# Kernel optimization log

Measured on AMD Instinct MI355X. Metric: run time of the kernel, lower is better.

The kernel has to match this reference:

```python
import jax, jax.numpy as jnp
import numpy as np

N = 1_000_000          # points
C_IN = 10              # decorated point features
C_OUT = 64             # pillar feature channels
S = 30_000             # number of pillars (segments)
EPS = 1e-3             # BatchNorm1d eps


def setup_inputs() -> dict:
    key = jax.random.key(0)
    ks = jax.random.split(key, 8)
    inputs = jax.random.normal(ks[0], (N, C_IN), dtype=jnp.float32)
    # every pillar gets ~N/S points; sorted, all segments non-empty
    unq_inv = jnp.sort(jnp.arange(N, dtype=jnp.int32) % S)
    W_lin = jax.random.normal(ks[1], (C_OUT, C_IN), dtype=jnp.float32) * 0.3
    gamma = 1.0 + 0.1 * jax.random.normal(ks[2], (C_OUT,), dtype=jnp.float32)
    beta = 0.1 * jax.random.normal(ks[3], (C_OUT,), dtype=jnp.float32)
    dw1 = jax.random.normal(ks[4], (C_OUT,), dtype=jnp.float32) * 0.5      # depthwise 1x1 conv (groups=C)
    pw1 = jax.random.normal(ks[5], (C_OUT, C_OUT), dtype=jnp.float32) * 0.1  # pointwise 1x1 conv
    dw2 = jax.random.normal(ks[6], (C_OUT,), dtype=jnp.float32) * 0.5
    pw2 = jax.random.normal(ks[7], (C_OUT, C_OUT), dtype=jnp.float32) * 0.1
    return {"inputs": inputs, "unq_inv": unq_inv, "W_lin": W_lin,
            "gamma": gamma, "beta": beta, "dw1": dw1, "pw1": pw1,
            "dw2": dw2, "pw2": pw2}


def reference(inputs, unq_inv, W_lin, gamma, beta, dw1, pw1, dw2, pw2):
    # Linear (no bias) -> BN (training-mode batch stats) -> ReLU
    x = inputs @ W_lin.T                                   # [N, C]
    mu = jnp.mean(x, axis=0)
    var = jnp.mean(jnp.square(x - mu), axis=0)             # biased var, as torch BN
    x = (x - mu) * jax.lax.rsqrt(var + EPS) * gamma + beta
    x = jax.nn.relu(x)

    # MAFF attention: local branch (depthwise scale -> swish -> 1x1 conv)
    s = x * dw1                                            # groups=C 1x1 conv == per-channel scale
    xl = (s * jax.nn.sigmoid(s)) @ pw1.T                   # [N, C]
    # global branch: avg-pool over points -> depthwise scale -> relu -> 1x1 conv
    g = jnp.mean(x, axis=0)                                # [C]
    xg = pw2 @ jax.nn.relu(dw2 * g)                        # [C]
    wei = jax.nn.sigmoid(xl + xg)                          # broadcast [N,C] + [C]
    xi = x * (1.0 + wei)

    # segment reductions keyed by pillar id (scatter_max + scatter_sum)
    x_max = jax.ops.segment_max(xi, unq_inv, num_segments=S,
                                indices_are_sorted=True)
    x_sum = jax.ops.segment_sum(xi, unq_inv, num_segments=S,
                                indices_are_sorted=True)
    return x_max + x_sum                                   # [S, C]
```

## Files before the change

kernel.cpp:

```cpp
#include <hip/hip_runtime.h>
#include <math.h>

#define N_PTS   1000000
#define CI      10
#define C       64
#define NSEG    30000
#define BN_EPS  1e-3f
#define FROFF   31104


using f32x4 = __attribute__((ext_vector_type(4))) float;
using s16x8 = __attribute__((ext_vector_type(8))) short;

__device__ inline short f2bf(float x) {
    unsigned u = __float_as_uint(x);
    unsigned r = (u + 0x7fffu + ((u >> 16) & 1u)) >> 16;
    return (short)r;
}
__device__ inline unsigned pack_trunc(float lo, float hi) {
    return (__float_as_uint(hi) & 0xffff0000u) | (__float_as_uint(lo) >> 16);
}
__device__ inline float frcp(float x) { return __builtin_amdgcn_rcpf(x); }
__device__ inline void lds_fence() {
    asm volatile("s_waitcnt lgkmcnt(0)" ::: "memory");
}

__global__ void __launch_bounds__(256) k_moments(const float* __restrict__ inp,
                                                 const int* __restrict__ idx,
                                                 float* __restrict__ ws,
                                                 int* __restrict__ starts) {
    const int tid = threadIdx.x;
    float v[65];
#pragma unroll
    for (int k = 0; k < 65; ++k) v[k] = 0.f;

    for (int p = blockIdx.x * blockDim.x + tid; p < N_PTS; p += gridDim.x * blockDim.x) {
        const float2* r2 = (const float2*)(inp + (size_t)p * CI);
        float2 a0 = r2[0], a1 = r2[1], a2 = r2[2], a3 = r2[3], a4 = r2[4];
        float r[CI] = {a0.x, a0.y, a1.x, a1.y, a2.x, a2.y, a3.x, a3.y, a4.x, a4.y};
#pragma unroll
        for (int i = 0; i < CI; ++i) v[i] += r[i];
        int kk = 10;
#pragma unroll
        for (int i = 0; i < CI; ++i)
#pragma unroll
            for (int j = i; j < CI; ++j) { v[kk] = fmaf(r[i], r[j], v[kk]); ++kk; }

        int iv = idx[p];
        if (p == 0) starts[0] = 0;
        else if (idx[p - 1] != iv) starts[iv] = p;
    }

#pragma unroll
    for (int k = 0; k < 65; ++k) {
#pragma unroll
        for (int off = 32; off >= 1; off >>= 1)
            v[k] += __shfl_xor(v[k], off, 64);
    }
    __shared__ float red[4 * 65];
    const int wv = tid >> 6, ln = tid & 63;
    if (ln == 0) {
#pragma unroll
        for (int k = 0; k < 65; ++k) red[wv * 65 + k] = v[k];
    }
    __syncthreads();
    if (tid < 65)
        atomicAdd(&ws[tid], red[tid] + red[65 + tid] + red[130 + tid] + red[195 + tid]);
}

__global__ void __launch_bounds__(256) k_gstats(const float* __restrict__ inp,
                                                const float* __restrict__ W,
                                                const float* __restrict__ gamma,
                                                const float* __restrict__ beta,
                                                float* __restrict__ ws) {
    const int tid  = threadIdx.x;
    const int wv   = tid >> 6;
    const int lane = tid & 63;
    const int m = lane & 15;
    const int q = lane >> 4;

    __shared__ float wp[C * CI];
    __shared__ float bsh[C];

    if (tid < C) {
        const int c = tid;
        float w[CI];
#pragma unroll
        for (int i = 0; i < CI; ++i) w[i] = W[c * CI + i];
        const float inv_n = 1.f / (float)N_PTS;

        float mu = 0.f;
#pragma unroll
        for (int i = 0; i < CI; ++i) mu = fmaf(w[i], ws[i], mu);
        mu *= inv_n;

        float ex2 = 0.f;
        int kk = 10;
#pragma unroll
        for (int i = 0; i < CI; ++i)
#pragma unroll
            for (int j = i; j < CI; ++j) {
                float mm = ws[kk];
                float t = w[i] * w[j] * mm;
                ex2 += (i == j) ? t : 2.f * t;
                ++kk;
            }
        ex2 *= inv_n;

        float var = ex2 - mu * mu;
        float rstd = rsqrtf(var + BN_EPS);
        float a = rstd * gamma[c];
        float b = beta[c] - mu * a;
        bsh[c] = b;
#pragma unroll
        for (int i = 0; i < CI; ++i) wp[c * CI + i] = a * w[i];
    }
    __syncthreads();

    s16x8 wfr[4];
#pragma unroll
    for (int nt = 0; nt < 4; ++nt) {
        s16x8 t;
#pragma unroll
        for (int j = 0; j < 8; ++j) {
            int k = 8 * q + j;
            t[j] = (k < CI) ? f2bf(wp[(nt * 16 + m) * CI + k]) : (short)0;
        }
        wfr[nt] = t;
    }
    float bb[4];
#pragma unroll
    for (int nt = 0; nt < 4; ++nt) bb[nt] = bsh[nt * 16 + m];

    const int wid = blockIdx.x * 4 + wv;
    const int nw  = gridDim.x * 4;
    const int NB  = N_PTS / 16;

    float2 P0, P1, P2, P3;
    auto loadrows = [&](int pb) {
        const float* row = inp + (size_t)(pb + m) * CI;
        if (q == 0) {
            P0 = *(const float2*)(row);     P1 = *(const float2*)(row + 2);
            P2 = *(const float2*)(row + 4); P3 = *(const float2*)(row + 6);
        } else if (q == 1) {
            P0 = *(const float2*)(row + 8);
        }
    };
    P0 = P1 = P2 = P3 = make_float2(0.f, 0.f);

    float sm[4] = {0.f, 0.f, 0.f, 0.f};
    const f32x4 zero = {0.f, 0.f, 0.f, 0.f};

    if (wid < NB) loadrows(wid * 16);
    for (int b = wid; b < NB; b += nw) {
        float2 L0 = P0, L1 = P1, L2 = P2, L3 = P3;
        if (b + nw < NB) loadrows((b + nw) * 16);

        union { s16x8 v; unsigned u[4]; } t;
        t.v = s16x8{0, 0, 0, 0, 0, 0, 0, 0};
        if (q < 2) t.u[0] = pack_trunc(L0.x, L0.y);
        if (q == 0) {
            t.u[1] = pack_trunc(L1.x, L1.y);
            t.u[2] = pack_trunc(L2.x, L2.y);
            t.u[3] = pack_trunc(L3.x, L3.y);
        }

        f32x4 xt[4];
#pragma unroll
        for (int nt = 0; nt < 4; ++nt) {
            xt[nt] = __builtin_amdgcn_mfma_f32_16x16x32_bf16(t.v, wfr[nt], zero, 0, 0, 0);
#pragma unroll
            for (int r = 0; r < 4; ++r)
                sm[nt] += fmaxf(xt[nt][r] + bb[nt], 0.f);
        }
    }

#pragma unroll
    for (int nt = 0; nt < 4; ++nt) {
        sm[nt] += __shfl_xor(sm[nt], 16, 64);
        sm[nt] += __shfl_xor(sm[nt], 32, 64);
    }
    float S = sm[0];
    if (q == 1) S = sm[1];
    if (q == 2) S = sm[2];
    if (q == 3) S = sm[3];

    __shared__ float red[4 * 64];
    red[wv * 64 + lane] = S;
    __syncthreads();
    if (tid < 64)
        atomicAdd(&ws[256 + tid], red[tid] + red[64 + tid] + red[128 + tid] + red[192 + tid]);
}

__global__ void k_prep(const float* __restrict__ W,
                       const float* __restrict__ gamma,
                       const float* __restrict__ beta,
                       const float* __restrict__ dw1,
                       const float* __restrict__ pw1,
                       const float* __restrict__ dw2,
                       const float* __restrict__ pw2,
                       float* __restrict__ ws) {
    const int lane = threadIdx.x;
    const int m = lane & 15, q = lane >> 4;
    const float inv_n = 1.f / (float)N_PTS;

    __shared__ float WP[C * CI];
    __shared__ float BSH[C], T[C], XG[C];

    {
        float w[CI];
#pragma unroll
        for (int i = 0; i < CI; ++i) w[i] = W[lane * CI + i];
        float mu = 0.f;
#pragma unroll
        for (int i = 0; i < CI; ++i) mu = fmaf(w[i], ws[i], mu);
        mu *= inv_n;
        float ex2 = 0.f;
        int kk = 10;
#pragma unroll
        for (int i = 0; i < CI; ++i)
#pragma unroll
            for (int j = i; j < CI; ++j) {
                float mm = ws[kk];
                float t = w[i] * w[j] * mm;
                ex2 += (i == j) ? t : 2.f * t;
                ++kk;
            }
        ex2 *= inv_n;
        float var = ex2 - mu * mu;
        float rstd = rsqrtf(var + BN_EPS);
        float a = rstd * gamma[lane];
        BSH[lane] = beta[lane] - mu * a;
#pragma unroll
        for (int i = 0; i < CI; ++i) WP[lane * CI + i] = a * w[i];
        T[lane] = fmaxf(dw2[lane] * (ws[256 + lane] * inv_n), 0.f);
    }
    __syncthreads();

    {
        float acc = 0.f;
#pragma unroll
        for (int k = 0; k < C; ++k) acc = fmaf(pw2[lane * C + k], T[k], acc);
        XG[lane] = acc;
    }
    __syncthreads();

    float4* FR = (float4*)(ws + FROFF);
    union { float4 f; s16x8 v; } u;

#pragma unroll
    for (int nt = 0; nt < 4; ++nt) {
        s16x8 tt;
#pragma unroll
        for (int j = 0; j < 8; ++j) {
            int k = 8 * q + j;
            tt[j] = (k < CI) ? f2bf(WP[(nt * 16 + m) * CI + k]) : (short)0;
        }
        u.v = tt; FR[nt * 64 + lane] = u.f;
    }
#pragma unroll
    for (int nt = 0; nt < 4; ++nt)
#pragma unroll
        for (int kc = 0; kc < 2; ++kc) {
            const float* src = pw1 + (nt * 16 + m) * C + kc * 32 + q * 8;
            float4 p0 = *(const float4*)src, p1 = *(const float4*)(src + 4);
            s16x8 tt;
            tt[0] = f2bf(p0.x); tt[1] = f2bf(p0.y); tt[2] = f2bf(p0.z); tt[3] = f2bf(p0.w);
            tt[4] = f2bf(p1.x); tt[5] = f2bf(p1.y); tt[6] = f2bf(p1.z); tt[7] = f2bf(p1.w);
            u.v = tt; FR[(4 + nt * 2 + kc) * 64 + lane] = u.f;
        }
    float4 f;
    f.x = BSH[m]; f.y = BSH[16 + m]; f.z = BSH[32 + m]; f.w = BSH[48 + m];
    FR[12 * 64 + lane] = f;
    f.x = dw1[m]; f.y = dw1[16 + m]; f.z = dw1[32 + m]; f.w = dw1[48 + m];
    FR[13 * 64 + lane] = f;
    f.x = XG[m]; f.y = XG[16 + m]; f.z = XG[32 + m]; f.w = XG[48 + m];
    FR[14 * 64 + lane] = f;
}

#define LD 68
#define SEGW 2
struct Rows { float2 r0, r1, r2, r3; };
__global__ void __launch_bounds__(128) k_main(const float* __restrict__ inp,
                                              const float* __restrict__ ws,
                                              const int* __restrict__ starts,
                                              float* __restrict__ out) {
    const int tid  = threadIdx.x;
    const int wv   = tid >> 6;
    const int lane = tid & 63;
    const int m = lane & 15;
    const int q = lane >> 4;
    const f32x4 zero = {0.f, 0.f, 0.f, 0.f};

    const float4* FR = (const float4*)(ws + FROFF);
    union { float4 f; s16x8 v; } u;
    s16x8 wfr[4];
#pragma unroll
    for (int nt = 0; nt < 4; ++nt) { u.f = FR[nt * 64 + lane]; wfr[nt] = u.v; }
    s16x8 bfr[4][2];
#pragma unroll
    for (int nt = 0; nt < 4; ++nt)
#pragma unroll
        for (int kc = 0; kc < 2; ++kc) { u.f = FR[(4 + nt * 2 + kc) * 64 + lane]; bfr[nt][kc] = u.v; }
    const float4 bb4  = FR[12 * 64 + lane];
    const float4 d14  = FR[13 * 64 + lane];
    const float4 xg4  = FR[14 * 64 + lane];
    const float bb[4]  = {bb4.x, bb4.y, bb4.z, bb4.w};
    const float d1v[4] = {d14.x, d14.y, d14.z, d14.w};
    const float xgv[4] = {xg4.x, xg4.y, xg4.z, xg4.w};

    __shared__ float sb[2][16 * LD];
    float* my = sb[wv];

    const int w  = blockIdx.x * 2 + wv;
    const int s0 = w * SEGW;

    int st1 = starts[s0 + 1];
    int st2 = (s0 + 2 < NSEG) ? starts[s0 + 2] : N_PTS;
    const int start   = starts[s0];
    const int end_all = st2;

    int cur = s0;
    int end_cur = st1;

    float sm[4]  = {0.f, 0.f, 0.f, 0.f};
    float mxv[4] = {-INFINITY, -INFINITY, -INFINITY, -INFINITY};

    auto flushseg = [&](int s) {
#pragma unroll
        for (int nt = 0; nt < 4; ++nt) {
            sm[nt] += __shfl_xor(sm[nt], 16, 64);
            sm[nt] += __shfl_xor(sm[nt], 32, 64);
            mxv[nt] = fmaxf(mxv[nt], __shfl_xor(mxv[nt], 16, 64));
            mxv[nt] = fmaxf(mxv[nt], __shfl_xor(mxv[nt], 32, 64));
        }
        float S = sm[0], M = mxv[0];
        if (q == 1) { S = sm[1]; M = mxv[1]; }
        if (q == 2) { S = sm[2]; M = mxv[2]; }
        if (q == 3) { S = sm[3]; M = mxv[3]; }
        out[(size_t)s * C + lane] = S + M;
#pragma unroll
        for (int nt = 0; nt < 4; ++nt) { sm[nt] = 0.f; mxv[nt] = -INFINITY; }
    };

    auto loadrows = [&](int pb) -> Rows {
        Rows R;
        R.r0 = R.r1 = R.r2 = R.r3 = make_float2(0.f, 0.f);
        const float* row = inp + (size_t)min(pb + m, N_PTS - 1) * CI;
        if (q == 0) {
            R.r0 = *(const float2*)(row);     R.r1 = *(const float2*)(row + 2);
            R.r2 = *(const float2*)(row + 4); R.r3 = *(const float2*)(row + 6);
        } else if (q == 1) {
            R.r0 = *(const float2*)(row + 8);
        }
        return R;
    };

    Rows A = loadrows(start);
    Rows B = (start + 16 < end_all) ? loadrows(start + 16) : A;

    for (int base = start; base < end_all; base += 16) {
        Rows L = A;
        A = B;
        if (base + 32 < end_all) B = loadrows(base + 32);

        const int nb = min(16, end_all - base);

        union { s16x8 v; unsigned u[4]; } t;
        t.v = s16x8{0, 0, 0, 0, 0, 0, 0, 0};
        if (q < 2) t.u[0] = pack_trunc(L.r0.x, L.r0.y);
        if (q == 0) {
            t.u[1] = pack_trunc(L.r1.x, L.r1.y);
            t.u[2] = pack_trunc(L.r2.x, L.r2.y);
            t.u[3] = pack_trunc(L.r3.x, L.r3.y);
        }

        f32x4 xt[4];
#pragma unroll
        for (int nt = 0; nt < 4; ++nt)
            xt[nt] = __builtin_amdgcn_mfma_f32_16x16x32_bf16(t.v, wfr[nt], zero, 0, 0, 0);

        float xn[4][4];
#pragma unroll
        for (int nt = 0; nt < 4; ++nt)
#pragma unroll
            for (int r = 0; r < 4; ++r) {
                float x = fmaxf(xt[nt][r] + bb[nt], 0.f);
                xn[nt][r] = x;
                float sg = x * d1v[nt];
                float sw = sg * frcp(1.f + __expf(-sg));
                my[(4 * q + r) * LD + nt * 16 + m] = sw;
            }
        lds_fence();

        s16x8 av[2];
#pragma unroll
        for (int kc = 0; kc < 2; ++kc) {
            const float* src = &my[m * LD + kc * 32 + q * 8];
            float4 p0 = *(const float4*)src;
            float4 p1 = *(const float4*)(src + 4);
            union { s16x8 v; unsigned u[4]; } tt;
            tt.u[0] = pack_trunc(p0.x, p0.y);
            tt.u[1] = pack_trunc(p0.z, p0.w);
            tt.u[2] = pack_trunc(p1.x, p1.y);
            tt.u[3] = pack_trunc(p1.z, p1.w);
            av[kc] = tt.v;
        }

        f32x4 xi[4];
#pragma unroll
        for (int nt = 0; nt < 4; ++nt) {
            xi[nt] = __builtin_amdgcn_mfma_f32_16x16x32_bf16(av[0], bfr[nt][0], zero, 0, 0, 0);
            xi[nt] = __builtin_amdgcn_mfma_f32_16x16x32_bf16(av[1], bfr[nt][1], xi[nt], 0, 0, 0);
        }
        lds_fence();

#pragma unroll
        for (int nt = 0; nt < 4; ++nt)
#pragma unroll
            for (int r = 0; r < 4; ++r) {
                float v   = xi[nt][r] + xgv[nt];
                float wei = frcp(1.f + __expf(-v));
                float x   = xn[nt][r];
                xi[nt][r] = fmaf(x, wei, x);
            }

        const int fin = base + nb;
        if (fin <= end_cur) {
            if (nb == 16) {
#pragma unroll
                for (int nt = 0; nt < 4; ++nt)
#pragma unroll
                    for (int r = 0; r < 4; ++r) {
                        sm[nt] += xi[nt][r];
                        mxv[nt] = fmaxf(mxv[nt], xi[nt][r]);
                    }
            } else {
#pragma unroll
                for (int nt = 0; nt < 4; ++nt)
#pragma unroll
                    for (int r = 0; r < 4; ++r) {
                        bool act = (4 * q + r) < nb;
                        sm[nt] += act ? xi[nt][r] : 0.f;
                        mxv[nt] = fmaxf(mxv[nt], act ? xi[nt][r] : -INFINITY);
                    }
            }
            if (fin == end_cur) { flushseg(cur); ++cur; end_cur = st2; }
        } else {
            const int B = end_cur - base;
#pragma unroll
            for (int nt = 0; nt < 4; ++nt)
#pragma unroll
                for (int r = 0; r < 4; ++r) {
                    bool act = (4 * q + r) < B;
                    sm[nt] += act ? xi[nt][r] : 0.f;
                    mxv[nt] = fmaxf(mxv[nt], act ? xi[nt][r] : -INFINITY);
                }
            flushseg(cur); ++cur;
#pragma unroll
            for (int nt = 0; nt < 4; ++nt)
#pragma unroll
                for (int r = 0; r < 4; ++r) {
                    int pt = 4 * q + r;
                    bool act = (pt >= B) && (pt < nb);
                    sm[nt] += act ? xi[nt][r] : 0.f;
                    mxv[nt] = fmaxf(mxv[nt], act ? xi[nt][r] : -INFINITY);
                }
            end_cur = st2;
        }
    }
}

extern "C" void kernel_launch(void* const* d_in, const int* in_sizes, int n_in,
                              void* d_out, int out_size, void* d_ws, size_t ws_size,
                              hipStream_t stream) {
    const float* inp   = (const float*)d_in[0];
    const int*   unq   = (const int*)d_in[1];
    const float* W     = (const float*)d_in[2];
    const float* gamma = (const float*)d_in[3];
    const float* beta  = (const float*)d_in[4];
    const float* dw1   = (const float*)d_in[5];
    const float* pw1   = (const float*)d_in[6];
    const float* dw2   = (const float*)d_in[7];
    const float* pw2   = (const float*)d_in[8];
    float* out = (float*)d_out;
    float* ws  = (float*)d_ws;
    int* starts = (int*)ws + 1024;

    hipMemsetAsync(ws, 0, 384 * sizeof(float), stream);

    k_moments <<<1024, 256, 0, stream>>>(inp, unq, ws, starts);
    k_gstats  <<<1024, 256, 0, stream>>>(inp, W, gamma, beta, ws);
    k_prep    <<<1,    64,  0, stream>>>(W, gamma, beta, dw1, pw1, dw2, pw2, ws);
    k_main    <<<7500, 128, 0, stream>>>(inp, ws, starts, out);
}
```

Measured before the change: 268.2 us.

## Replace atomic reductions with per-block partials and two-stage reductions

The moments and global-stats kernels now write per-block partial sums to workspace instead of using atomicAdd. A separate reduction kernel sums the moment partials, and the prep kernel, widened to 1024 threads, sums the gstats partials. This removes the memset and the atomic contention. Separately, the grids grow to 2048 blocks, k_moments processes two points per thread with float4 loads, k_gstats uses double-buffered prefetch, and one LDS fence in k_main is dropped. In exchange it adds an extra kernel launch, and dropping the fence risks an LDS race.

```diff
diff --git a/kernel.cpp b/kernel.cpp
--- a/kernel.cpp
+++ b/kernel.cpp
@@ -6,7 +6,13 @@
 #define C       64
 #define NSEG    30000
 #define BN_EPS  1e-3f
-#define FROFF   31104
+
+#define NBLK_M  2048
+#define NBLK_G  2048
+#define P1STR   72
+#define P1OFF   32768
+#define P2OFF   (P1OFF + NBLK_M * P1STR)
+#define FROFF   (P2OFF + NBLK_G * 64)
 
 
 using f32x4 = __attribute__((ext_vector_type(4))) float;
@@ -23,6 +29,11 @@
 __device__ inline float frcp(float x) { return __builtin_amdgcn_rcpf(x); }
 __device__ inline void lds_fence() {
     asm volatile("s_waitcnt lgkmcnt(0)" ::: "memory");
+}
+
+struct Rows { float2 r0, r1, r2, r3; };
+__device__ inline Rows zrows() {
+    Rows R; R.r0 = R.r1 = R.r2 = R.r3 = make_float2(0.f, 0.f); return R;
 }
 
 __global__ void __launch_bounds__(256) k_moments(const float* __restrict__ inp,
@@ -34,21 +45,29 @@
 #pragma unroll
     for (int k = 0; k < 65; ++k) v[k] = 0.f;
 
-    for (int p = blockIdx.x * blockDim.x + tid; p < N_PTS; p += gridDim.x * blockDim.x) {
-        const float2* r2 = (const float2*)(inp + (size_t)p * CI);
-        float2 a0 = r2[0], a1 = r2[1], a2 = r2[2], a3 = r2[3], a4 = r2[4];
-        float r[CI] = {a0.x, a0.y, a1.x, a1.y, a2.x, a2.y, a3.x, a3.y, a4.x, a4.y};
-#pragma unroll
-        for (int i = 0; i < CI; ++i) v[i] += r[i];
+    const int NPP = N_PTS / 2;
+    for (int pp = blockIdx.x * blockDim.x + tid; pp < NPP; pp += gridDim.x * blockDim.x) {
+        const float4* base = (const float4*)(inp + (size_t)pp * 20);
+        float4 a = base[0], b4 = base[1], c = base[2], d = base[3], e = base[4];
+        float r0[CI] = {a.x, a.y, a.z, a.w, b4.x, b4.y, b4.z, b4.w, c.x, c.y};
+        float r1[CI] = {c.z, c.w, d.x, d.y, d.z, d.w, e.x, e.y, e.z, e.w};
+#pragma unroll
+        for (int i = 0; i < CI; ++i) v[i] += r0[i] + r1[i];
         int kk = 10;
 #pragma unroll
         for (int i = 0; i < CI; ++i)
 #pragma unroll
-            for (int j = i; j < CI; ++j) { v[kk] = fmaf(r[i], r[j], v[kk]); ++kk; }
-
-        int iv = idx[p];
-        if (p == 0) starts[0] = 0;
-        else if (idx[p - 1] != iv) starts[iv] = p;
+            for (int j = i; j < CI; ++j) {
+                v[kk] = fmaf(r0[i], r0[j], v[kk]);
+                v[kk] = fmaf(r1[i], r1[j], v[kk]);
+                ++kk;
+            }
+
+        const int p0 = 2 * pp;
+        int2 iv = *(const int2*)(idx + p0);
+        if (p0 == 0) starts[0] = 0;
+        else { int prev = idx[p0 - 1]; if (prev != iv.x) starts[iv.x] = p0; }
+        if (iv.x != iv.y) starts[iv.y] = p0 + 1;
     }
 
 #pragma unroll
@@ -65,7 +84,24 @@
     }
     __syncthreads();
     if (tid < 65)
-        atomicAdd(&ws[tid], red[tid] + red[65 + tid] + red[130 + tid] + red[195 + tid]);
+        ws[P1OFF + blockIdx.x * P1STR + tid] =
+            red[tid] + red[65 + tid] + red[130 + tid] + red[195 + tid];
+}
+
+__global__ void __launch_bounds__(256) k_red(float* __restrict__ ws) {
+    const int k = blockIdx.x;
+    float s = 0.f;
+    for (int i = threadIdx.x; i < NBLK_M; i += 256)
+        s += ws[P1OFF + i * P1STR + k];
+    __shared__ float r[256];
+    r[threadIdx.x] = s;
+    __syncthreads();
+#pragma unroll
+    for (int off = 128; off > 0; off >>= 1) {
+        if (threadIdx.x < off) r[threadIdx.x] += r[threadIdx.x + off];
+        __syncthreads();
+    }
+    if (threadIdx.x == 0) ws[k] = r[0];
 }
 
 __global__ void __launch_bounds__(256) k_gstats(const float* __restrict__ inp,
@@ -78,6 +114,7 @@
     const int lane = tid & 63;
     const int m = lane & 15;
     const int q = lane >> 4;
+    const float inv_n = 1.f / (float)N_PTS;
 
     __shared__ float wp[C * CI];
     __shared__ float bsh[C];
@@ -87,13 +124,10 @@
         float w[CI];
 #pragma unroll
         for (int i = 0; i < CI; ++i) w[i] = W[c * CI + i];
-        const float inv_n = 1.f / (float)N_PTS;
-
         float mu = 0.f;
 #pragma unroll
         for (int i = 0; i < CI; ++i) mu = fmaf(w[i], ws[i], mu);
         mu *= inv_n;
-
         float ex2 = 0.f;
         int kk = 10;
 #pragma unroll
@@ -106,12 +140,10 @@
                 ++kk;
             }
         ex2 *= inv_n;
-
         float var = ex2 - mu * mu;
         float rstd = rsqrtf(var + BN_EPS);
         float a = rstd * gamma[c];
-        float b = beta[c] - mu * a;
-        bsh[c] = b;
+        bsh[c] = beta[c] - mu * a;
 #pragma unroll
         for (int i = 0; i < CI; ++i) wp[c * CI + i] = a * w[i];
     }
@@ -132,46 +164,53 @@
 #pragma unroll
     for (int nt = 0; nt < 4; ++nt) bb[nt] = bsh[nt * 16 + m];
 
-    const int wid = blockIdx.x * 4 + wv;
-    const int nw  = gridDim.x * 4;
-    const int NB  = N_PTS / 16;
-
-    float2 P0, P1, P2, P3;
-    auto loadrows = [&](int pb) {
+    auto loadrows = [&](int pb) -> Rows {
+        Rows R = zrows();
         const float* row = inp + (size_t)(pb + m) * CI;
         if (q == 0) {
-            P0 = *(const float2*)(row);     P1 = *(const float2*)(row + 2);
-            P2 = *(const float2*)(row + 4); P3 = *(const float2*)(row + 6);
+            R.r0 = *(const float2*)(row);     R.r1 = *(const float2*)(row + 2);
+            R.r2 = *(const float2*)(row + 4); R.r3 = *(const float2*)(row + 6);
         } else if (q == 1) {
-            P0 = *(const float2*)(row + 8);
-        }
+            R.r0 = *(const float2*)(row + 8);
+        }
+        return R;
     };
-    P0 = P1 = P2 = P3 = make_float2(0.f, 0.f);
+    auto mkfrag = [&](const Rows& L) -> s16x8 {
+        union { s16x8 v; unsigned u[4]; } t;
+        t.v = s16x8{0, 0, 0, 0, 0, 0, 0, 0};
+        if (q < 2) t.u[0] = pack_trunc(L.r0.x, L.r0.y);
+        if (q == 0) {
+            t.u[1] = pack_trunc(L.r1.x, L.r1.y);
+            t.u[2] = pack_trunc(L.r2.x, L.r2.y);
+            t.u[3] = pack_trunc(L.r3.x, L.r3.y);
+        }
+        return t.v;
+    };
+
+    const int wid = blockIdx.x * 4 + wv;
+    const int STR = NBLK_G * 4;
+    const int NB  = N_PTS / 16;
 
     float sm[4] = {0.f, 0.f, 0.f, 0.f};
     const f32x4 zero = {0.f, 0.f, 0.f, 0.f};
 
-    if (wid < NB) loadrows(wid * 16);
-    for (int b = wid; b < NB; b += nw) {
-        float2 L0 = P0, L1 = P1, L2 = P2, L3 = P3;
-        if (b + nw < NB) loadrows((b + nw) * 16);
-
-        union { s16x8 v; unsigned u[4]; } t;
-        t.v = s16x8{0, 0, 0, 0, 0, 0, 0, 0};
-        if (q < 2) t.u[0] = pack_trunc(L0.x, L0.y);
-        if (q == 0) {
-            t.u[1] = pack_trunc(L1.x, L1.y);
-            t.u[2] = pack_trunc(L2.x, L2.y);
-            t.u[3] = pack_trunc(L3.x, L3.y);
-        }
-
-        f32x4 xt[4];
+    Rows Pf0 = zrows(), Pf1 = zrows();
+    if (wid < NB) Pf0 = loadrows(wid * 16);
+    if (wid + STR < NB) Pf1 = loadrows((wid + STR) * 16);
+    int j = 0;
+    for (int i = wid; i < NB; i += STR, ++j) {
+        Rows L = (j & 1) ? Pf1 : Pf0;
+        if (i + 2 * STR < NB) {
+            if (j & 1) Pf1 = loadrows((i + 2 * STR) * 16);
+            else       Pf0 = loadrows((i + 2 * STR) * 16);
+        }
+        s16x8 t = mkfrag(L);
 #pragma unroll
         for (int nt = 0; nt < 4; ++nt) {
-            xt[nt] = __builtin_amdgcn_mfma_f32_16x16x32_bf16(t.v, wfr[nt], zero, 0, 0, 0);
+            f32x4 xt = __builtin_amdgcn_mfma_f32_16x16x32_bf16(t, wfr[nt], zero, 0, 0, 0);
 #pragma unroll
             for (int r = 0; r < 4; ++r)
-                sm[nt] += fmaxf(xt[nt][r] + bb[nt], 0.f);
+                sm[nt] += fmaxf(xt[r] + bb[nt], 0.f);
         }
     }
 
@@ -189,28 +228,44 @@
     red[wv * 64 + lane] = S;
     __syncthreads();
     if (tid < 64)
-        atomicAdd(&ws[256 + tid], red[tid] + red[64 + tid] + red[128 + tid] + red[192 + tid]);
-}
-
-__global__ void k_prep(const float* __restrict__ W,
-                       const float* __restrict__ gamma,
-                       const float* __restrict__ beta,
-                       const float* __restrict__ dw1,
-                       const float* __restrict__ pw1,
-                       const float* __restrict__ dw2,
-                       const float* __restrict__ pw2,
-                       float* __restrict__ ws) {
-    const int lane = threadIdx.x;
-    const int m = lane & 15, q = lane >> 4;
+        ws[P2OFF + blockIdx.x * 64 + tid] =
+            red[tid] + red[64 + tid] + red[128 + tid] + red[192 + tid];
+}
+
+__global__ void __launch_bounds__(1024) k_prep(const float* __restrict__ W,
+                                               const float* __restrict__ gamma,
+                                               const float* __restrict__ beta,
+                                               const float* __restrict__ dw1,
+                                               const float* __restrict__ pw1,
+                                               const float* __restrict__ dw2,
+                                               const float* __restrict__ pw2,
+                                               float* __restrict__ ws) {
+    const int tid = threadIdx.x;
+    const int c = tid & 63, g = tid >> 6;
     const float inv_n = 1.f / (float)N_PTS;
 
-    __shared__ float WP[C * CI];
-    __shared__ float BSH[C], T[C], XG[C];
+    __shared__ float R[1024];
+    __shared__ float GS[C], WP[C * CI], BSH[C], T[C], XG[C];
 
     {
+        float s = 0.f;
+        for (int i = g; i < NBLK_G; i += 16)
+            s += ws[P2OFF + i * 64 + c];
+        R[tid] = s;
+    }
+    __syncthreads();
+    if (g == 0) {
+        float t = 0.f;
+#pragma unroll
+        for (int gg = 0; gg < 16; ++gg) t += R[gg * 64 + c];
+        GS[c] = t;
+    }
+    __syncthreads();
+
+    if (tid < C) {
         float w[CI];
 #pragma unroll
-        for (int i = 0; i < CI; ++i) w[i] = W[lane * CI + i];
+        for (int i = 0; i < CI; ++i) w[i] = W[tid * CI + i];
         float mu = 0.f;
 #pragma unroll
         for (int i = 0; i < CI; ++i) mu = fmaf(w[i], ws[i], mu);
@@ -229,58 +284,59 @@
         ex2 *= inv_n;
         float var = ex2 - mu * mu;
         float rstd = rsqrtf(var + BN_EPS);
-        float a = rstd * gamma[lane];
-        BSH[lane] = beta[lane] - mu * a;
-#pragma unroll
-        for (int i = 0; i < CI; ++i) WP[lane * CI + i] = a * w[i];
-        T[lane] = fmaxf(dw2[lane] * (ws[256 + lane] * inv_n), 0.f);
-    }
-    __syncthreads();
-
-    {
+        float a = rstd * gamma[tid];
+        BSH[tid] = beta[tid] - mu * a;
+#pragma unroll
+        for (int i = 0; i < CI; ++i) WP[tid * CI + i] = a * w[i];
+        T[tid] = fmaxf(dw2[tid] * (GS[tid] * inv_n), 0.f);
+    }
+    __syncthreads();
+
+    if (tid < C) {
         float acc = 0.f;
 #pragma unroll
-        for (int k = 0; k < C; ++k) acc = fmaf(pw2[lane * C + k], T[k], acc);
-        XG[lane] = acc;
-    }
-    __syncthreads();
-
-    float4* FR = (float4*)(ws + FROFF);
-    union { float4 f; s16x8 v; } u;
-
-#pragma unroll
-    for (int nt = 0; nt < 4; ++nt) {
-        s16x8 tt;
-#pragma unroll
-        for (int j = 0; j < 8; ++j) {
-            int k = 8 * q + j;
-            tt[j] = (k < CI) ? f2bf(WP[(nt * 16 + m) * CI + k]) : (short)0;
-        }
-        u.v = tt; FR[nt * 64 + lane] = u.f;
-    }
-#pragma unroll
-    for (int nt = 0; nt < 4; ++nt)
-#pragma unroll
-        for (int kc = 0; kc < 2; ++kc) {
-            const float* src = pw1 + (nt * 16 + m) * C + kc * 32 + q * 8;
-            float4 p0 = *(const float4*)src, p1 = *(const float4*)(src + 4);
+        for (int k = 0; k < C; ++k) acc = fmaf(pw2[tid * C + k], T[k], acc);
+        XG[tid] = acc;
+    }
+    __syncthreads();
+
+    if (tid < C) {
+        const int lane = tid, m = lane & 15, q = lane >> 4;
+        float4* FR = (float4*)(ws + FROFF);
+        union { float4 f; s16x8 v; } u;
+#pragma unroll
+        for (int nt = 0; nt < 4; ++nt) {
             s16x8 tt;
-            tt[0] = f2bf(p0.x); tt[1] = f2bf(p0.y); tt[2] = f2bf(p0.z); tt[3] = f2bf(p0.w);
-            tt[4] = f2bf(p1.x); tt[5] = f2bf(p1.y); tt[6] = f2bf(p1.z); tt[7] = f2bf(p1.w);
-            u.v = tt; FR[(4 + nt * 2 + kc) * 64 + lane] = u.f;
-        }
-    float4 f;
-    f.x = BSH[m]; f.y = BSH[16 + m]; f.z = BSH[32 + m]; f.w = BSH[48 + m];
-    FR[12 * 64 + lane] = f;
-    f.x = dw1[m]; f.y = dw1[16 + m]; f.z = dw1[32 + m]; f.w = dw1[48 + m];
-    FR[13 * 64 + lane] = f;
-    f.x = XG[m]; f.y = XG[16 + m]; f.z = XG[32 + m]; f.w = XG[48 + m];
-    FR[14 * 64 + lane] = f;
+#pragma unroll
+            for (int j = 0; j < 8; ++j) {
+                int k = 8 * q + j;
+                tt[j] = (k < CI) ? f2bf(WP[(nt * 16 + m) * CI + k]) : (short)0;
+            }
+            u.v = tt; FR[nt * 64 + lane] = u.f;
+        }
+#pragma unroll
+        for (int nt = 0; nt < 4; ++nt)
+#pragma unroll
+            for (int kc = 0; kc < 2; ++kc) {
+                const float* src = pw1 + (nt * 16 + m) * C + kc * 32 + q * 8;
+                float4 p0 = *(const float4*)src, p1 = *(const float4*)(src + 4);
+                s16x8 tt;
+                tt[0] = f2bf(p0.x); tt[1] = f2bf(p0.y); tt[2] = f2bf(p0.z); tt[3] = f2bf(p0.w);
+                tt[4] = f2bf(p1.x); tt[5] = f2bf(p1.y); tt[6] = f2bf(p1.z); tt[7] = f2bf(p1.w);
+                u.v = tt; FR[(4 + nt * 2 + kc) * 64 + lane] = u.f;
+            }
+        float4 f;
+        f.x = BSH[m]; f.y = BSH[16 + m]; f.z = BSH[32 + m]; f.w = BSH[48 + m];
+        FR[12 * 64 + lane] = f;
+        f.x = dw1[m]; f.y = dw1[16 + m]; f.z = dw1[32 + m]; f.w = dw1[48 + m];
+        FR[13 * 64 + lane] = f;
+        f.x = XG[m]; f.y = XG[16 + m]; f.z = XG[32 + m]; f.w = XG[48 + m];
+        FR[14 * 64 + lane] = f;
+    }
 }
 
 #define LD 68
 #define SEGW 2
-struct Rows { float2 r0, r1, r2, r3; };
 __global__ void __launch_bounds__(128) k_main(const float* __restrict__ inp,
                                               const float* __restrict__ ws,
                                               const int* __restrict__ starts,
@@ -344,8 +400,7 @@
     };
 
     auto loadrows = [&](int pb) -> Rows {
-        Rows R;
-        R.r0 = R.r1 = R.r2 = R.r3 = make_float2(0.f, 0.f);
+        Rows R = zrows();
         const float* row = inp + (size_t)min(pb + m, N_PTS - 1) * CI;
         if (q == 0) {
             R.r0 = *(const float2*)(row);     R.r1 = *(const float2*)(row + 2);
@@ -355,17 +410,7 @@
         }
         return R;
     };
-
-    Rows A = loadrows(start);
-    Rows B = (start + 16 < end_all) ? loadrows(start + 16) : A;
-
-    for (int base = start; base < end_all; base += 16) {
-        Rows L = A;
-        A = B;
-        if (base + 32 < end_all) B = loadrows(base + 32);
-
-        const int nb = min(16, end_all - base);
-
+    auto mkfrag = [&](const Rows& L) -> s16x8 {
         union { s16x8 v; unsigned u[4]; } t;
         t.v = s16x8{0, 0, 0, 0, 0, 0, 0, 0};
         if (q < 2) t.u[0] = pack_trunc(L.r0.x, L.r0.y);
@@ -374,11 +419,24 @@
             t.u[2] = pack_trunc(L.r2.x, L.r2.y);
             t.u[3] = pack_trunc(L.r3.x, L.r3.y);
         }
-
+        return t.v;
+    };
+
+    Rows PA = loadrows(start);
+    Rows PB = (start + 16 < end_all) ? loadrows(start + 16) : PA;
+
+    for (int base = start; base < end_all; base += 16) {
+        Rows L = PA;
+        PA = PB;
+        if (base + 32 < end_all) PB = loadrows(base + 32);
+
+        const int nb = min(16, end_all - base);
+
+        s16x8 t = mkfrag(L);
         f32x4 xt[4];
 #pragma unroll
         for (int nt = 0; nt < 4; ++nt)
-            xt[nt] = __builtin_amdgcn_mfma_f32_16x16x32_bf16(t.v, wfr[nt], zero, 0, 0, 0);
+            xt[nt] = __builtin_amdgcn_mfma_f32_16x16x32_bf16(t, wfr[nt], zero, 0, 0, 0);
 
         float xn[4][4];
 #pragma unroll
@@ -413,7 +471,6 @@
             xi[nt] = __builtin_amdgcn_mfma_f32_16x16x32_bf16(av[0], bfr[nt][0], zero, 0, 0, 0);
             xi[nt] = __builtin_amdgcn_mfma_f32_16x16x32_bf16(av[1], bfr[nt][1], xi[nt], 0, 0, 0);
         }
-        lds_fence();
 
 #pragma unroll
         for (int nt = 0; nt < 4; ++nt)
@@ -487,10 +544,9 @@
     float* ws  = (float*)d_ws;
     int* starts = (int*)ws + 1024;
 
-    hipMemsetAsync(ws, 0, 384 * sizeof(float), stream);
-
-    k_moments <<<1024, 256, 0, stream>>>(inp, unq, ws, starts);
-    k_gstats  <<<1024, 256, 0, stream>>>(inp, W, gamma, beta, ws);
-    k_prep    <<<1,    64,  0, stream>>>(W, gamma, beta, dw1, pw1, dw2, pw2, ws);
-    k_main    <<<7500, 128, 0, stream>>>(inp, ws, starts, out);
-}
+    k_moments <<<NBLK_M, 256, 0, stream>>>(inp, unq, ws, starts);
+    k_red     <<<65,     256, 0, stream>>>(ws);
+    k_gstats  <<<NBLK_G, 256, 0, stream>>>(inp, W, gamma, beta, ws);
+    k_prep    <<<1,     1024, 0, stream>>>(W, gamma, beta, dw1, pw1, dw2, pw2, ws);
+    k_main    <<<7500,   128, 0, stream>>>(inp, ws, starts, out);
+}
```

Result: slower. 294.8 us (+9.9%).
